# Optimization experiments

Hardware: AMD Instinct MI355X
Metric: run time of the kernel (lower is better)

Reference implementation:

```python
import jax, jax.numpy as jnp
import numpy as np

B, N, C, D = 16, 2048, 256, 256


def setup_inputs() -> dict:
    key = jax.random.key(0)
    ks = jax.random.split(key, 8)
    x = jax.random.normal(ks[0], (B, N, C), dtype=jnp.float32)
    valid_len = jax.random.randint(ks[1], (B,), 0, N)
    # nn.Linear params: weight [out, in], bias [out]
    s = 1.0 / np.sqrt(C)
    Wq = jax.random.uniform(ks[2], (D, C), dtype=jnp.float32, minval=-s, maxval=s)
    bq = jax.random.uniform(ks[3], (D,), dtype=jnp.float32, minval=-s, maxval=s)
    Wk = jax.random.uniform(ks[4], (D, C), dtype=jnp.float32, minval=-s, maxval=s)
    bk = jax.random.uniform(ks[5], (D,), dtype=jnp.float32, minval=-s, maxval=s)
    Wv = jax.random.uniform(ks[6], (D, C), dtype=jnp.float32, minval=-s, maxval=s)
    bv = jax.random.uniform(ks[7], (D,), dtype=jnp.float32, minval=-s, maxval=s)
    return {"x": x, "valid_len": valid_len, "Wq": Wq, "bq": bq,
            "Wk": Wk, "bk": bk, "Wv": Wv, "bv": bv}


def reference(x, valid_len, Wq, bq, Wk, bk, Wv, bv):
    # QKV projections (nn.Linear: x @ W^T + b)
    q = jnp.einsum('bnc,dc->bnd', x, Wq) + bq
    k = jnp.einsum('bnc,dc->bnd', x, Wk) + bk
    v = jnp.einsum('bnc,dc->bnd', x, Wv) + bv
    # scores [B, N, N] = q @ k^T (no scaling: scale_factor_d unused in forward)
    scores = jnp.einsum('bnd,bmd->bnm', q, k)
    # key-side valid-length mask: arange(N) < valid_len[b], broadcast over queries
    mask = jnp.arange(N)[None, :] < valid_len[:, None]          # [B, N]
    scores = jnp.where(mask[:, None, :], scores, jnp.float32(-1000000.0))
    attn = jax.nn.softmax(scores, axis=-1)
    return jnp.einsum('bnm,bmd->bnd', attn, v)
```

## Files before the change

### kernel.cpp

```cpp
#include <hip/hip_runtime.h>
#include <hip/hip_bf16.h>
#include <stdint.h>

typedef __attribute__((ext_vector_type(8))) _Float16 half8;
typedef __attribute__((ext_vector_type(4))) _Float16 half4;
typedef __attribute__((ext_vector_type(2))) __fp16 fp16x2;
typedef __attribute__((ext_vector_type(4))) float f32x4;
typedef __attribute__((ext_vector_type(16))) float f32x16;
typedef __attribute__((ext_vector_type(4))) float float4v;

#define DEVI static __device__ __forceinline__

constexpr int Bb = 16, Nn = 2048, Cc = 256, Dd = 256;

DEVI unsigned short f2h_bits(float f) {
  _Float16 h = (_Float16)f;
  union { _Float16 h; unsigned short u; } c;
  c.h = h;
  return c.u;
}

DEVI void gl_lds16(const void* gsrc, void* ldst) {
  __builtin_amdgcn_global_load_lds(
      (const __attribute__((address_space(1))) unsigned int*)gsrc,
      (__attribute__((address_space(3))) unsigned int*)ldst, 16, 0, 0);
}

DEVI f32x4 mfma16h(half8 a, half8 b, f32x4 c) {
  return __builtin_amdgcn_mfma_f32_16x16x32_f16(a, b, c, 0, 0, 0);
}
DEVI f32x16 mfma32h(half8 a, half8 b, f32x16 c) {
  return __builtin_amdgcn_mfma_f32_32x32x16_f16(a, b, c, 0, 0, 0);
}

DEVI unsigned int pkrtz(float a, float b) {
  union { fp16x2 h; unsigned int u; } c;
  c.h = __builtin_amdgcn_cvt_pkrtz(a, b);
  return c.u;
}

__global__ void k_split(const float* __restrict__ x, const float* __restrict__ wq,
                        const float* __restrict__ wk, const float* __restrict__ wv,
                        _Float16* __restrict__ xh, _Float16* __restrict__ wh) {
  int i = blockIdx.x * 256 + threadIdx.x;
  if (i < 2097152) {
    float4v v = reinterpret_cast<const float4v*>(x)[i];
    half4 h;
#pragma unroll
    for (int j = 0; j < 4; ++j) h[j] = (_Float16)v[j];
    reinterpret_cast<half4*>(xh)[i] = h;
  } else {
    int ii = i - 2097152;
    int mat = ii >> 16;
    int rem = ii & 65535;
    const float* w = (mat == 0) ? wq : ((mat == 1) ? wk : wv);
    wh[(size_t)mat * 65536 + rem] = (_Float16)w[rem];
  }
}

__global__ __launch_bounds__(256, 2) void k_qkv(
    const _Float16* __restrict__ xh, const _Float16* __restrict__ wh,
    const float* __restrict__ bq, const float* __restrict__ bk, const float* __restrict__ bv,
    _Float16* __restrict__ qout, _Float16* __restrict__ kout, _Float16* __restrict__ vt) {
  __shared__ __align__(16) unsigned short smem[17408];

  const int tid = threadIdx.x;
  const int m0 = blockIdx.x * 128;
  const int n0 = blockIdx.y * 128;
  const int mat = blockIdx.z;
  const _Float16* wmat = wh + (size_t)mat * 65536;
  const int wave = tid >> 6, lane = tid & 63;
  const int wr = wave >> 1, wc = wave & 1;
  const int l15 = lane & 15, lq = lane >> 4;

  f32x4 zero4 = {0.f, 0.f, 0.f, 0.f};
  f32x4 acc[4][4];
#pragma unroll
  for (int a = 0; a < 4; ++a)
#pragma unroll
    for (int b2 = 0; b2 < 4; ++b2) acc[a][b2] = zero4;

  char* As = (char*)smem;
  char* Bs = (char*)smem + 16384;

  for (int kc = 0; kc < 4; ++kc) {
#pragma unroll
    for (int i = 0; i < 4; ++i) {
      int p = i * 4096 + tid * 16;
      int row = p >> 7;
      int src_in_row = (p & 127) ^ ((row & 7) << 4);
      const char* g = (const char*)(xh + (size_t)(m0 + row) * Cc + kc * 64) + src_in_row;
      gl_lds16(g, As + p);
    }
#pragma unroll
    for (int i = 0; i < 4; ++i) {
      int p = i * 4096 + tid * 16;
      int row = p >> 7;
      int src_in_row = (p & 127) ^ ((row & 7) << 4);
      const char* g = (const char*)(wmat + (size_t)(n0 + row) * Cc + kc * 64) + src_in_row;
      gl_lds16(g, Bs + p);
    }
    __syncthreads();
#pragma unroll
    for (int ks = 0; ks < 2; ++ks) {
      half8 af[4], bfr[4];
#pragma unroll
      for (int mf = 0; mf < 4; ++mf) {
        int row = wr * 64 + mf * 16 + l15;
        int byte = (row * 128 + ks * 64 + lq * 16) ^ ((row & 7) << 4);
        af[mf] = *(const half8*)(As + byte);
      }
#pragma unroll
      for (int nf = 0; nf < 4; ++nf) {
        int row = wc * 64 + nf * 16 + l15;
        int byte = (row * 128 + ks * 64 + lq * 16) ^ ((row & 7) << 4);
        bfr[nf] = *(const half8*)(Bs + byte);
      }
#pragma unroll
      for (int mf = 0; mf < 4; ++mf)
#pragma unroll
        for (int nf = 0; nf < 4; ++nf) acc[mf][nf] = mfma16h(af[mf], bfr[nf], acc[mf][nf]);
    }
    __syncthreads();
  }

  const float* bias = (mat == 0) ? bq : ((mat == 1) ? bk : bv);
  if (mat < 2) {
    _Float16* oo = (mat == 0) ? qout : kout;
#pragma unroll
    for (int nf = 0; nf < 4; ++nf) {
      int col = n0 + wc * 64 + nf * 16 + l15;
      float bval = bias[col];
#pragma unroll
      for (int mf = 0; mf < 4; ++mf) {
        int grow = m0 + wr * 64 + mf * 16 + lq * 4;
#pragma unroll
        for (int r = 0; r < 4; ++r)
          oo[(size_t)(grow + r) * Dd + col] = (_Float16)(acc[mf][nf][r] + bval);
      }
    }
  } else {
    __syncthreads();
#pragma unroll
    for (int nf = 0; nf < 4; ++nf) {
      int dl = wc * 64 + nf * 16 + l15;
      float bval = bias[n0 + dl];
#pragma unroll
      for (int mf = 0; mf < 4; ++mf) {
        int nl = wr * 64 + mf * 16 + lq * 4;
#pragma unroll
        for (int r = 0; r < 4; ++r) smem[dl * 136 + nl + r] = f2h_bits(acc[mf][nf][r] + bval);
      }
    }
    __syncthreads();
    const int bbat = m0 >> 11, tok0 = m0 & 2047;
#pragma unroll
    for (int pss = 0; pss < 8; ++pss) {
      int idx = pss * 256 + tid;
      int dl = idx >> 4;
      int cu = idx & 15;
      half8 vval = *(const half8*)((const char*)smem + dl * 272 + cu * 16);
      size_t off = ((size_t)bbat * Dd + n0 + dl) * Nn + tok0 + cu * 8;
      *(half8*)(vt + off) = vval;
    }
  }
}

__global__ void k_order(const int* __restrict__ vlen, int* __restrict__ order) {
  __shared__ int nts[512];
  int t = threadIdx.x;
  int b = t >> 5, kh = t & 1;
  int L = vlen[b];
  int Lk = (L == 0) ? Nn : L;
  int avail = Lk - kh * 1024;
  int nt = (avail > 0) ? ((avail + 63) >> 6) : 0;
  nt = nt > 16 ? 16 : nt;
  nts[t] = nt;
  __syncthreads();
  int rank = 0;
  for (int j = 0; j < 512; ++j) {
    int nj = nts[j];
    if (nj > nt || (nj == nt && j < t)) ++rank;
  }
  order[rank] = t;
}

__global__ __launch_bounds__(512, 2) void k_attn_f(
    const _Float16* __restrict__ qg, const _Float16* __restrict__ kin,
    const _Float16* __restrict__ vt, const int* __restrict__ vlen,
    const int* __restrict__ order, _Float16* __restrict__ Op,
    float* __restrict__ ml) {
  __shared__ __align__(16) char SMEM[149504];
  char* const KVb = SMEM;
  unsigned int* const PL = (unsigned int*)(SMEM + 131072);
  float* const mex = (float*)(SMEM + 147456);
  float* const lex = (float*)(SMEM + 148480);

  const int tid = threadIdx.x;
  const int wave = tid >> 6, lane = tid & 63;
  const int l31 = lane & 31, h = lane >> 5;
  const int wq = wave >> 1, wk = wave & 1;

  for (int s = 0; s < 2; ++s) {
    const int item = order[s == 0 ? blockIdx.x : (511 - blockIdx.x)];
    const int b = item >> 5;
    const int q0 = ((item >> 1) & 15) * 128;
    const int kh = item & 1;
    const int kst = kh * 1024;
    const int L = vlen[b];
    const bool uni = (L == 0);
    const int Lk = uni ? Nn : L;
    const int avail = Lk - kst;
    int nt = (avail > 0) ? ((avail + 63) >> 6) : 0;
    nt = nt > 16 ? 16 : nt;
    const size_t prow = (size_t)(b * 2 + kh) * Nn + q0;

    if (nt == 0) {
      if (tid < 128) {
        ml[(prow + tid) * 2 + 0] = -1e30f;
        ml[(prow + tid) * 2 + 1] = 0.f;
      }
      continue;
    }

    const char* kbase = (const char*)(kin + (size_t)b * Nn * Dd);
    const char* vbase = (const char*)(vt + (size_t)b * Dd * Nn);
    const char* qbase = (const char*)(qg + ((size_t)b * Nn + q0) * Dd);

    auto STAGE = [&](int buf, int t) {
      char* dst = KVb + buf * 65536;
      const int k0 = kst + t * 64;
#pragma unroll
      for (int i = 0; i < 4; ++i) {
        int p = i * 8192 + tid * 16;
        int row = p >> 9;
        int sl = ((p & 511) >> 4) ^ (row & 31);
        gl_lds16(kbase + (size_t)(k0 + row) * 512 + (sl << 4), dst + p);
      }
#pragma unroll
      for (int i = 0; i < 4; ++i) {
        int p = i * 8192 + tid * 16;
        int r = p >> 9;
        int sl = ((p & 511) >> 4) ^ (r & 31);
        int cl = sl << 4;
        int d = r * 4 + (cl >> 7);
        int kbyte = cl & 127;
        gl_lds16(vbase + (size_t)d * (Nn * 2) + (size_t)k0 * 2 + kbyte, dst + 32768 + p);
      }
    };

    STAGE(0, 0);
#pragma unroll
    for (int i = 0; i < 8; ++i) {
      int p = i * 8192 + tid * 16;
      int row = p >> 9;
      int sl = ((p & 511) >> 4) ^ (row & 31);
      gl_lds16(qbase + (size_t)row * 512 + (sl << 4), KVb + 65536 + p);
    }
    asm volatile("s_waitcnt vmcnt(0)" ::: "memory");
    asm volatile("s_barrier" ::: "memory");

    half8 qreg[16];
    {
      const int row = wq * 32 + l31;
#pragma unroll
      for (int kt = 0; kt < 16; ++kt) {
        int byte = row * 512 + (((kt * 2 + h) ^ (row & 31)) << 4);
        qreg[kt] = *(const half8*)(KVb + 65536 + byte);
      }
    }
    asm volatile("s_waitcnt lgkmcnt(0)" ::: "memory");
    asm volatile("s_barrier" ::: "memory");

    f32x16 acc[4];
#pragma unroll
    for (int dg = 0; dg < 4; ++dg)
#pragma unroll
      for (int r = 0; r < 16; ++r) acc[dg][r] = 0.f;
    float m = -__builtin_inff();
    float lsum = 0.f;

    for (int t = 0; t < nt; ++t) {
      const int cur = t & 1;
      if (t + 1 < nt) {
        STAGE(cur ^ 1, t + 1);
        asm volatile("s_waitcnt vmcnt(8)" ::: "memory");
      } else {
        asm volatile("s_waitcnt vmcnt(0)" ::: "memory");
      }
      asm volatile("s_barrier" ::: "memory");

      const char* Ks = KVb + cur * 65536;
      const char* Vs = Ks + 32768;
      const int k0 = kst + t * 64;

      f32x16 st;
#pragma unroll
      for (int r = 0; r < 16; ++r) st[r] = 0.f;
      if (!uni) {
        const int key = wk * 32 + l31;
        __builtin_amdgcn_s_setprio(1);
#pragma unroll
        for (int kt = 0; kt < 16; ++kt) {
          int byte = key * 512 + (((kt * 2 + h) ^ l31) << 4);
          half8 kf = *(const half8*)(Ks + byte);
          st = mfma32h(kf, qreg[kt], st);
        }
        __builtin_amdgcn_s_setprio(0);
        if (k0 + 64 > L) {
#pragma unroll
          for (int r = 0; r < 16; ++r) {
            int keyg = k0 + wk * 32 + (r & 3) + 8 * (r >> 2) + 4 * h;
            if (keyg >= L) st[r] = -1e6f;
          }
        }
      }

      float pm = st[0];
#pragma unroll
      for (int r = 1; r < 16; ++r) pm = fmaxf(pm, st[r]);
      pm = fmaxf(pm, __shfl_xor(pm, 32));
      if (lane < 32) mex[wave * 32 + lane] = pm;
      asm volatile("s_waitcnt lgkmcnt(0)\ns_barrier" ::: "memory");
      float pmo = mex[(wave ^ 1) * 32 + l31];
      float mnew = fmaxf(m, fmaxf(pm, pmo));
      float scale = __expf(m - mnew);
      m = mnew;
      float psum = 0.f;
#pragma unroll
      for (int r = 0; r < 16; ++r) {
        float p_ = __expf(st[r] - mnew);
        st[r] = p_;
        psum += p_;
      }
      lsum = lsum * scale + psum;

#pragma unroll
      for (int i = 0; i < 8; ++i) {
        unsigned int pk = pkrtz(st[2 * i], st[2 * i + 1]);
        int kp = wk * 16 + 4 * (i >> 1) + (i & 1) + 2 * h;
        PL[wq * 1024 + kp * 32 + l31] = pk;
      }
      asm volatile("s_waitcnt lgkmcnt(0)\ns_barrier" ::: "memory");

      union { unsigned int u[4]; half8 v; } pf0, pf1, pf2, pf3;
#pragma unroll
      for (int w = 0; w < 4; ++w) {
        pf0.u[w] = PL[wq * 1024 + (0 * 8 + h * 4 + w) * 32 + l31];
        pf1.u[w] = PL[wq * 1024 + (1 * 8 + h * 4 + w) * 32 + l31];
        pf2.u[w] = PL[wq * 1024 + (2 * 8 + h * 4 + w) * 32 + l31];
        pf3.u[w] = PL[wq * 1024 + (3 * 8 + h * 4 + w) * 32 + l31];
      }

#pragma unroll
      for (int dg = 0; dg < 4; ++dg)
#pragma unroll
        for (int r = 0; r < 16; ++r) acc[dg][r] *= scale;

      __builtin_amdgcn_s_setprio(1);
#pragma unroll
      for (int dg = 0; dg < 4; ++dg) {
        int r = wk * 32 + dg * 8 + (l31 >> 2);
#pragma unroll
        for (int ks = 0; ks < 4; ++ks) {
          int slot = (l31 & 3) * 8 + ks * 2 + h;
          half8 vf = *(const half8*)(Vs + r * 512 + ((slot ^ (r & 31)) << 4));
          acc[dg] = mfma32h(vf, ks == 0 ? pf0.v : (ks == 1 ? pf1.v : (ks == 2 ? pf2.v : pf3.v)),
                            acc[dg]);
        }
      }
      __builtin_amdgcn_s_setprio(0);

      asm volatile("s_barrier" ::: "memory");
    }

    lsum += __shfl_xor(lsum, 32);
    if (lane < 32) lex[wave * 32 + lane] = lsum;
    asm volatile("s_waitcnt lgkmcnt(0)\ns_barrier" ::: "memory");
    float ltot = lsum + lex[(wave ^ 1) * 32 + l31];
    float linv = 1.f / ltot;

    if (h == 0 && wk == 0) {
      size_t qq = prow + wq * 32 + l31;
      ml[qq * 2 + 0] = m;
      ml[qq * 2 + 1] = ltot;
    }

    _Float16* T = (_Float16*)SMEM;
    {
      const int ql = wq * 32 + l31;
#pragma unroll
      for (int dg = 0; dg < 4; ++dg)
#pragma unroll
        for (int r = 0; r < 16; ++r) {
          int d = wk * 128 + dg * 32 + (r & 3) + 8 * (r >> 2) + 4 * h;
          T[ql * 264 + d] = (_Float16)(acc[dg][r] * linv);
        }
    }
    asm volatile("s_waitcnt lgkmcnt(0)\ns_barrier" ::: "memory");

    {
      const int rb = tid >> 6;
      const int c4 = (tid & 63) * 4;
#pragma unroll
      for (int i = 0; i < 16; ++i) {
        int row = rb + i * 8;
        half4 v = *(const half4*)(T + row * 264 + c4);
        *(half4*)(Op + (prow + row) * Dd + c4) = v;
      }
    }
    asm volatile("s_waitcnt lgkmcnt(0)\ns_barrier" ::: "memory");
  }
}

__global__ __launch_bounds__(256) void k_comb(const _Float16* __restrict__ Op,
                                              const float* __restrict__ ml,
                                              float* __restrict__ out) {
  int rid = blockIdx.x * 4 + (threadIdx.x >> 6);
  int lane = threadIdx.x & 63;
  int b = rid >> 11, q = rid & 2047;
  size_t i0 = (size_t)(b * 2 + 0) * Nn + q;
  size_t i1 = (size_t)(b * 2 + 1) * Nn + q;
  float m0 = ml[i0 * 2], l0 = ml[i0 * 2 + 1];
  float m1 = ml[i1 * 2], l1 = ml[i1 * 2 + 1];
  float M = fmaxf(m0, m1);
  float c0 = (l0 > 0.f) ? __expf(m0 - M) * l0 : 0.f;
  float c1 = (l1 > 0.f) ? __expf(m1 - M) * l1 : 0.f;
  float inv = 1.f / (c0 + c1);
  c0 *= inv;
  c1 *= inv;
  float4v o = {0.f, 0.f, 0.f, 0.f};
  if (c0 > 0.f) {
    half4 o0 = *(const half4*)(Op + i0 * 256 + lane * 4);
#pragma unroll
    for (int j = 0; j < 4; ++j) o[j] = c0 * (float)o0[j];
  }
  if (c1 > 0.f) {
    half4 o1 = *(const half4*)(Op + i1 * 256 + lane * 4);
#pragma unroll
    for (int j = 0; j < 4; ++j) o[j] += c1 * (float)o1[j];
  }
  *(float4v*)(out + ((size_t)b * Nn + q) * 256 + lane * 4) = o;
}

__global__ __launch_bounds__(512, 2) void k_attn(
    const _Float16* __restrict__ qg, const _Float16* __restrict__ kin,
    const _Float16* __restrict__ vt, const int* __restrict__ vlen,
    float* __restrict__ out) {
  __shared__ __align__(16) char SMEM[149504];
  char* const KVb = SMEM;
  unsigned int* const PL = (unsigned int*)(SMEM + 131072);
  float* const mex = (float*)(SMEM + 147456);
  float* const lex = (float*)(SMEM + 148480);

  const int tid = threadIdx.x;
  const int wave = tid >> 6, lane = tid & 63;
  const int l31 = lane & 31, h = lane >> 5;
  const int wq = wave >> 1, wk = wave & 1;
  const int id = blockIdx.x;
  const int g = id & 7;
  const int j = id >> 3;
  const int b = g + 8 * (j >> 4);
  const int q0 = (j & 15) * 128;
  const int L = vlen[b];
  const bool uni = (L == 0);
  const int Lk = uni ? Nn : L;
  const int nt = (Lk + 63) >> 6;

  const char* kbase = (const char*)(kin + (size_t)b * Nn * Dd);
  const char* vbase = (const char*)(vt + (size_t)b * Dd * Nn);
  const char* qbase = (const char*)(qg + ((size_t)b * Nn + q0) * Dd);

  auto STAGE = [&](int buf, int t) {
    char* dst = KVb + buf * 65536;
    const int k0 = t * 64;
#pragma unroll
    for (int i = 0; i < 4; ++i) {
      int p = i * 8192 + tid * 16;
      int row = p >> 9;
      int sl = ((p & 511) >> 4) ^ (row & 31);
      gl_lds16(kbase + (size_t)(k0 + row) * 512 + (sl << 4), dst + p);
    }
#pragma unroll
    for (int i = 0; i < 4; ++i) {
      int p = i * 8192 + tid * 16;
      int r = p >> 9;
      int sl = ((p & 511) >> 4) ^ (r & 31);
      int cl = sl << 4;
      int d = r * 4 + (cl >> 7);
      int kbyte = cl & 127;
      gl_lds16(vbase + (size_t)d * (Nn * 2) + (size_t)k0 * 2 + kbyte, dst + 32768 + p);
    }
  };

  STAGE(0, 0);
#pragma unroll
  for (int i = 0; i < 8; ++i) {
    int p = i * 8192 + tid * 16;
    int row = p >> 9;
    int sl = ((p & 511) >> 4) ^ (row & 31);
    gl_lds16(qbase + (size_t)row * 512 + (sl << 4), KVb + 65536 + p);
  }
  asm volatile("s_waitcnt vmcnt(0)" ::: "memory");
  asm volatile("s_barrier" ::: "memory");

  half8 qreg[16];
  {
    const int row = wq * 32 + l31;
#pragma unroll
    for (int kt = 0; kt < 16; ++kt) {
      int byte = row * 512 + (((kt * 2 + h) ^ (row & 31)) << 4);
      qreg[kt] = *(const half8*)(KVb + 65536 + byte);
    }
  }
  asm volatile("s_waitcnt lgkmcnt(0)" ::: "memory");
  asm volatile("s_barrier" ::: "memory");

  f32x16 acc[4];
#pragma unroll
  for (int dg = 0; dg < 4; ++dg)
#pragma unroll
    for (int r = 0; r < 16; ++r) acc[dg][r] = 0.f;
  float m = -__builtin_inff();
  float lsum = 0.f;

  for (int t = 0; t < nt; ++t) {
    const int cur = t & 1;
    if (t + 1 < nt) {
      STAGE(cur ^ 1, t + 1);
      asm volatile("s_waitcnt vmcnt(8)" ::: "memory");
    } else {
      asm volatile("s_waitcnt vmcnt(0)" ::: "memory");
    }
    asm volatile("s_barrier" ::: "memory");

    const char* Ks = KVb + cur * 65536;
    const char* Vs = Ks + 32768;
    const int k0 = t * 64;

    f32x16 st;
#pragma unroll
    for (int r = 0; r < 16; ++r) st[r] = 0.f;
    if (!uni) {
      const int key = wk * 32 + l31;
      __builtin_amdgcn_s_setprio(1);
#pragma unroll
      for (int kt = 0; kt < 16; ++kt) {
        int byte = key * 512 + (((kt * 2 + h) ^ l31) << 4);
        half8 kf = *(const half8*)(Ks + byte);
        st = mfma32h(kf, qreg[kt], st);
      }
      __builtin_amdgcn_s_setprio(0);
      if (k0 + 64 > L) {
#pragma unroll
        for (int r = 0; r < 16; ++r) {
          int keyg = k0 + wk * 32 + (r & 3) + 8 * (r >> 2) + 4 * h;
          if (keyg >= L) st[r] = -1e6f;
        }
      }
    }

    float pm = st[0];
#pragma unroll
    for (int r = 1; r < 16; ++r) pm = fmaxf(pm, st[r]);
    pm = fmaxf(pm, __shfl_xor(pm, 32));
    if (lane < 32) mex[wave * 32 + lane] = pm;
    asm volatile("s_waitcnt lgkmcnt(0)\ns_barrier" ::: "memory");
    float pmo = mex[(wave ^ 1) * 32 + l31];
    float mnew = fmaxf(m, fmaxf(pm, pmo));
    float scale = __expf(m - mnew);
    m = mnew;
    float psum = 0.f;
#pragma unroll
    for (int r = 0; r < 16; ++r) {
      float p_ = __expf(st[r] - mnew);
      st[r] = p_;
      psum += p_;
    }
    lsum = lsum * scale + psum;

#pragma unroll
    for (int i = 0; i < 8; ++i) {
      unsigned int pk = pkrtz(st[2 * i], st[2 * i + 1]);
      int kp = wk * 16 + 4 * (i >> 1) + (i & 1) + 2 * h;
      PL[wq * 1024 + kp * 32 + l31] = pk;
    }
    asm volatile("s_waitcnt lgkmcnt(0)\ns_barrier" ::: "memory");

    union { unsigned int u[4]; half8 v; } pf0, pf1, pf2, pf3;
#pragma unroll
    for (int w = 0; w < 4; ++w) {
      pf0.u[w] = PL[wq * 1024 + (0 * 8 + h * 4 + w) * 32 + l31];
      pf1.u[w] = PL[wq * 1024 + (1 * 8 + h * 4 + w) * 32 + l31];
      pf2.u[w] = PL[wq * 1024 + (2 * 8 + h * 4 + w) * 32 + l31];
      pf3.u[w] = PL[wq * 1024 + (3 * 8 + h * 4 + w) * 32 + l31];
    }

#pragma unroll
    for (int dg = 0; dg < 4; ++dg)
#pragma unroll
      for (int r = 0; r < 16; ++r) acc[dg][r] *= scale;

    __builtin_amdgcn_s_setprio(1);
#pragma unroll
    for (int dg = 0; dg < 4; ++dg) {
      int r = wk * 32 + dg * 8 + (l31 >> 2);
#pragma unroll
      for (int ks = 0; ks < 4; ++ks) {
        int slot = (l31 & 3) * 8 + ks * 2 + h;
        half8 vf = *(const half8*)(Vs + r * 512 + ((slot ^ (r & 31)) << 4));
        acc[dg] = mfma32h(vf, ks == 0 ? pf0.v : (ks == 1 ? pf1.v : (ks == 2 ? pf2.v : pf3.v)),
                          acc[dg]);
      }
    }
    __builtin_amdgcn_s_setprio(0);

    asm volatile("s_barrier" ::: "memory");
  }

  lsum += __shfl_xor(lsum, 32);
  if (lane < 32) lex[wave * 32 + lane] = lsum;
  asm volatile("s_waitcnt lgkmcnt(0)\ns_barrier" ::: "memory");
  float linv = 1.f / (lsum + lex[(wave ^ 1) * 32 + l31]);

  float* T = (float*)SMEM;
  {
    const int ql = wq * 32 + l31;
#pragma unroll
    for (int dg = 0; dg < 4; ++dg)
#pragma unroll
      for (int r = 0; r < 16; ++r) {
        int d = wk * 128 + dg * 32 + (r & 3) + 8 * (r >> 2) + 4 * h;
        T[ql * 260 + d] = acc[dg][r] * linv;
      }
  }
  asm volatile("s_waitcnt lgkmcnt(0)\ns_barrier" ::: "memory");

  {
    const int rb = tid >> 6;
    const int c4 = (tid & 63) * 4;
#pragma unroll
    for (int i = 0; i < 16; ++i) {
      int row = rb + i * 8;
      float4v v = *(const float4v*)(T + row * 260 + c4);
      *(float4v*)(out + ((size_t)b * Nn + q0 + row) * Dd + c4) = v;
    }
  }
}

extern "C" void kernel_launch(void* const* d_in, const int* in_sizes, int n_in,
                              void* d_out, int out_size, void* d_ws, size_t ws_size,
                              hipStream_t stream) {
  const float* x = (const float*)d_in[0];
  const int* vlen = (const int*)d_in[1];
  const float* Wq = (const float*)d_in[2];
  const float* bq = (const float*)d_in[3];
  const float* Wk = (const float*)d_in[4];
  const float* bk = (const float*)d_in[5];
  const float* Wv = (const float*)d_in[6];
  const float* bv = (const float*)d_in[7];
  float* out = (float*)d_out;
  char* ws = (char*)d_ws;

  _Float16* qh = (_Float16*)(ws);
  _Float16* kk = (_Float16*)(ws + 16777216);
  _Float16* vt = (_Float16*)(ws + 33554432);
  _Float16* wh = (_Float16*)(ws + 50331648);
  _Float16* Op = (_Float16*)(ws + 51380224);
  float* ml = (float*)(ws + 84934656);
  int* order = (int*)(ws + 85458944);
  _Float16* xh = (_Float16*)d_out;

  k_split<<<8960, 256, 0, stream>>>(x, Wq, Wk, Wv, xh, wh);
  k_qkv<<<dim3(256, 2, 3), 256, 0, stream>>>(xh, wh, bq, bk, bv, qh, kk, vt);
  if (ws_size >= 85460992ull) {
    k_order<<<1, 512, 0, stream>>>(vlen, order);
    k_attn_f<<<256, 512, 0, stream>>>(qh, kk, vt, vlen, order, Op, ml);
    k_comb<<<8192, 256, 0, stream>>>(Op, ml, out);
  } else {
    k_attn<<<256, 512, 0, stream>>>(qh, kk, vt, vlen, out);
  }
}
```

Measured before the change: 140.1 us.

## Fold work ordering into split kernel and group attention items by batch pairs

Removes the separate k_order launch by computing the attention schedule in an extra block of k_split. The new schedule pairs a long batch with a short batch into 8 groups, so each group of blocks (blockIdx & 7) handles items from only two batches, sorted by tile count. This is meant to improve L2 locality of K/V reuse across concurrently running blocks while keeping load balance. It also saves one kernel launch.

```diff
diff --git a/kernel.cpp b/kernel.cpp
--- a/kernel.cpp
+++ b/kernel.cpp
@@ -41,7 +41,45 @@
 
 __global__ void k_split(const float* __restrict__ x, const float* __restrict__ wq,
                         const float* __restrict__ wk, const float* __restrict__ wv,
-                        _Float16* __restrict__ xh, _Float16* __restrict__ wh) {
+                        const int* __restrict__ vlen, _Float16* __restrict__ xh,
+                        _Float16* __restrict__ wh, int* __restrict__ sched) {
+  __shared__ int ntb[16];
+  __shared__ int bofg[16];
+  if (blockIdx.x == 8960) {
+    int t = threadIdx.x;
+    if (t < 16) {
+      int L = vlen[t];
+      int Lk = (L == 0) ? Nn : L;
+      ntb[t] = (Lk + 63) >> 6;
+    }
+    __syncthreads();
+    if (t < 16) {
+      int r = 0;
+      for (int j = 0; j < 16; ++j)
+        if (ntb[j] > ntb[t] || (ntb[j] == ntb[t] && j < t)) ++r;
+      int g = (r < 8) ? r : 15 - r;
+      int lb = (r < 8) ? 0 : 1;
+      bofg[g * 2 + lb] = t;
+    }
+    __syncthreads();
+    for (int s = 0; s < 2; ++s) {
+      int ti = s * 256 + t;
+      int g = ti >> 6, li = ti & 63;
+      int lb = li >> 5, qi = (li >> 1) & 15, kh = li & 1;
+      int b = bofg[g * 2 + lb];
+      int full = ntb[b];
+      int myv = kh ? (full > 16 ? full - 16 : 0) : (full > 16 ? 16 : full);
+      int r = 0;
+      for (int j = 0; j < 64; ++j) {
+        int bj = bofg[g * 2 + (j >> 5)];
+        int fj = ntb[bj];
+        int vj = (j & 1) ? (fj > 16 ? fj - 16 : 0) : (fj > 16 ? 16 : fj);
+        if (vj > myv || (vj == myv && j < li)) ++r;
+      }
+      sched[g * 64 + r] = b * 32 + qi * 2 + kh;
+    }
+    return;
+  }
   int i = blockIdx.x * 256 + threadIdx.x;
   if (i < 2097152) {
     float4v v = reinterpret_cast<const float4v*>(x)[i];
@@ -166,29 +204,10 @@
   }
 }
 
-__global__ void k_order(const int* __restrict__ vlen, int* __restrict__ order) {
-  __shared__ int nts[512];
-  int t = threadIdx.x;
-  int b = t >> 5, kh = t & 1;
-  int L = vlen[b];
-  int Lk = (L == 0) ? Nn : L;
-  int avail = Lk - kh * 1024;
-  int nt = (avail > 0) ? ((avail + 63) >> 6) : 0;
-  nt = nt > 16 ? 16 : nt;
-  nts[t] = nt;
-  __syncthreads();
-  int rank = 0;
-  for (int j = 0; j < 512; ++j) {
-    int nj = nts[j];
-    if (nj > nt || (nj == nt && j < t)) ++rank;
-  }
-  order[rank] = t;
-}
-
 __global__ __launch_bounds__(512, 2) void k_attn_f(
     const _Float16* __restrict__ qg, const _Float16* __restrict__ kin,
     const _Float16* __restrict__ vt, const int* __restrict__ vlen,
-    const int* __restrict__ order, _Float16* __restrict__ Op,
+    const int* __restrict__ sched, _Float16* __restrict__ Op,
     float* __restrict__ ml) {
   __shared__ __align__(16) char SMEM[149504];
   char* const KVb = SMEM;
@@ -200,9 +219,11 @@
   const int wave = tid >> 6, lane = tid & 63;
   const int l31 = lane & 31, h = lane >> 5;
   const int wq = wave >> 1, wk = wave & 1;
+  const int g = blockIdx.x & 7;
+  const int slot = blockIdx.x >> 3;
 
   for (int s = 0; s < 2; ++s) {
-    const int item = order[s == 0 ? blockIdx.x : (511 - blockIdx.x)];
+    const int item = sched[g * 64 + (s == 0 ? slot : 63 - slot)];
     const int b = item >> 5;
     const int q0 = ((item >> 1) & 15) * 128;
     const int kh = item & 1;
@@ -363,8 +384,8 @@
         int r = wk * 32 + dg * 8 + (l31 >> 2);
 #pragma unroll
         for (int ks = 0; ks < 4; ++ks) {
-          int slot = (l31 & 3) * 8 + ks * 2 + h;
-          half8 vf = *(const half8*)(Vs + r * 512 + ((slot ^ (r & 31)) << 4));
+          int slotv = (l31 & 3) * 8 + ks * 2 + h;
+          half8 vf = *(const half8*)(Vs + r * 512 + ((slotv ^ (r & 31)) << 4));
           acc[dg] = mfma32h(vf, ks == 0 ? pf0.v : (ks == 1 ? pf1.v : (ks == 2 ? pf2.v : pf3.v)),
                             acc[dg]);
         }
@@ -607,8 +628,8 @@
       int r = wk * 32 + dg * 8 + (l31 >> 2);
 #pragma unroll
       for (int ks = 0; ks < 4; ++ks) {
-        int slot = (l31 & 3) * 8 + ks * 2 + h;
-        half8 vf = *(const half8*)(Vs + r * 512 + ((slot ^ (r & 31)) << 4));
+        int slotv = (l31 & 3) * 8 + ks * 2 + h;
+        half8 vf = *(const half8*)(Vs + r * 512 + ((slotv ^ (r & 31)) << 4));
         acc[dg] = mfma32h(vf, ks == 0 ? pf0.v : (ks == 1 ? pf1.v : (ks == 2 ? pf2.v : pf3.v)),
                           acc[dg]);
       }
@@ -668,14 +689,13 @@
   _Float16* wh = (_Float16*)(ws + 50331648);
   _Float16* Op = (_Float16*)(ws + 51380224);
   float* ml = (float*)(ws + 84934656);
-  int* order = (int*)(ws + 85458944);
+  int* sched = (int*)(ws + 85458944);
   _Float16* xh = (_Float16*)d_out;
 
-  k_split<<<8960, 256, 0, stream>>>(x, Wq, Wk, Wv, xh, wh);
+  k_split<<<8961, 256, 0, stream>>>(x, Wq, Wk, Wv, vlen, xh, wh, sched);
   k_qkv<<<dim3(256, 2, 3), 256, 0, stream>>>(xh, wh, bq, bk, bv, qh, kk, vt);
   if (ws_size >= 85460992ull) {
-    k_order<<<1, 512, 0, stream>>>(vlen, order);
-    k_attn_f<<<256, 512, 0, stream>>>(qh, kk, vt, vlen, order, Op, ml);
+    k_attn_f<<<256, 512, 0, stream>>>(qh, kk, vt, vlen, sched, Op, ml);
     k_comb<<<8192, 256, 0, stream>>>(Op, ml, out);
   } else {
     k_attn<<<256, 512, 0, stream>>>(qh, kk, vt, vlen, out);
```

Result: faster. 132.1 us (-5.7%).
